# Kernel optimization log

Measured on AMD Instinct MI355X. Metric: run time of the kernel, lower is better.

The kernel has to match this reference:

```python
import jax, jax.numpy as jnp
import numpy as np
import math

DIM_IN = 512
DIM_OUT = 512
KERNEL = 3
STYLE_DIM = 2 * 128
LIN_SCALE = 1.0 / math.sqrt(STYLE_DIM)      # EqualLinear scale (lr_mul=1)
CONV_SCALE = 1.0 / math.sqrt(DIM_IN * KERNEL ** 2)  # fan_in = dim_in * k**2 (as in source)
PAD = KERNEL // 2


def setup_inputs() -> dict:
    key = jax.random.key(0)
    ks = jax.random.split(key, 5)
    B, T = 16, 2048
    x = jax.random.normal(ks[0], (B, DIM_IN, T), dtype=jnp.float32)
    c_src = jax.random.normal(ks[1], (B, 128), dtype=jnp.float32)
    c_trg = jax.random.normal(ks[2], (B, 128), dtype=jnp.float32)
    style_w = jax.random.normal(ks[3], (DIM_IN, STYLE_DIM), dtype=jnp.float32)
    style_b = jnp.ones((DIM_IN,), dtype=jnp.float32)  # bias_init=1
    weight = jax.random.normal(ks[4], (1, DIM_OUT, DIM_IN, KERNEL), dtype=jnp.float32)
    return {"x": x, "c_src": c_src, "c_trg": c_trg,
            "style_w": style_w, "style_b": style_b, "weight": weight}


def reference(x, c_src, c_trg, style_w, style_b, weight):
    B = x.shape[0]
    # EqualLinear: style code s [B, dim_in]
    c = jnp.concatenate([c_src, c_trg], axis=-1)              # [B, 256]
    s = c @ (style_w * LIN_SCALE).T + style_b                 # [B, dim_in]
    # Modulate: w [B, dim_out, dim_in, k]
    w = CONV_SCALE * weight * s[:, None, :, None]
    # Demodulate over (dim_in, k)
    demod = jax.lax.rsqrt(jnp.sum(w * w, axis=(2, 3)) + 1e-8)  # [B, dim_out]
    w = w * demod[:, :, None, None]
    # Per-sample conv1d, padding 'same' (pad = k//2), vmapped over batch
    def conv1(xi, wi):
        # xi: [dim_in, T], wi: [dim_out, dim_in, k]
        out = jax.lax.conv_general_dilated(
            xi[None], wi, window_strides=(1,), padding=[(PAD, PAD)],
            dimension_numbers=("NCH", "OIH", "NCH"))
        return out[0]                                          # [dim_out, T]
    return jax.vmap(conv1)(x, w)                               # [B, dim_out, T]
```

## Files before the change

### kernel.cpp

```cpp
#include <hip/hip_runtime.h>
#include <cstdint>
#include <cstddef>


#define LIN_SCALE  0.0625f
#define CONV_SCALE 0.014731391f

#define B_   16
#define CIN  512
#define COUT 512
#define T_   2048
#define TP   2050

typedef __bf16 bf16x8 __attribute__((ext_vector_type(8)));
typedef float  f32x4  __attribute__((ext_vector_type(4)));
typedef unsigned short u16x8 __attribute__((ext_vector_type(8)));
typedef unsigned short u16x2 __attribute__((ext_vector_type(2)));

__device__ inline unsigned short f2bf(float f) {
  __bf16 h = (__bf16)f;
  return __builtin_bit_cast(unsigned short, h);
}

__global__ __launch_bounds__(256) void style_kernel(const float* __restrict__ c_src,
                                                    const float* __restrict__ c_trg,
                                                    const float* __restrict__ sw,
                                                    const float* __restrict__ sb,
                                                    float* __restrict__ s) {
  __shared__ float c[256];
  const int b = blockIdx.y;
  const int tid = threadIdx.x;
  c[tid] = (tid < 128) ? c_src[b * 128 + tid] : c_trg[b * 128 + tid - 128];
  __syncthreads();
  const int w = tid >> 6, lane = tid & 63;
  #pragma unroll
  for (int rr = 0; rr < 16; ++rr) {
    const int i = blockIdx.x * 64 + w * 16 + rr;
    const float* row = sw + (size_t)i * 256;
    float acc = row[lane] * c[lane] + row[lane + 64] * c[lane + 64]
              + row[lane + 128] * c[lane + 128] + row[lane + 192] * c[lane + 192];
    #pragma unroll
    for (int off = 32; off; off >>= 1) acc += __shfl_down(acc, off, 64);
    if (lane == 0) s[b * 512 + i] = acc * LIN_SCALE + sb[i];
  }
}

__global__ __launch_bounds__(256) void modw_kernel(const float* __restrict__ weight,
                                                   const float* __restrict__ s,
                                                   unsigned short* __restrict__ Wm) {
  const int o = blockIdx.x;
  const int tid = threadIdx.x;
  __shared__ float wsh[1536];
  __shared__ float svs[16 * 512];
  __shared__ float partial[16][4];
  __shared__ float demv[16];

  #pragma unroll
  for (int j = tid; j < 1536; j += 256) wsh[j] = weight[(size_t)o * 1536 + j];
  #pragma unroll
  for (int j = tid; j < 16 * 512; j += 256) svs[j] = s[j];
  __syncthreads();

  float wr[6];
  #pragma unroll
  for (int q = 0; q < 6; ++q) wr[q] = wsh[tid * 6 + q] * CONV_SCALE;

  const int lane = tid & 63, w = tid >> 6;
  float ssb[16];
  #pragma unroll
  for (int b = 0; b < 16; ++b) {
    const float s0 = svs[b * 512 + 2 * tid];
    const float s1 = svs[b * 512 + 2 * tid + 1];
    float ss = 0.f;
    #pragma unroll
    for (int q = 0; q < 3; ++q) { float v = wr[q] * s0; ss += v * v; }
    #pragma unroll
    for (int q = 3; q < 6; ++q) { float v = wr[q] * s1; ss += v * v; }
    ssb[b] = ss;
  }
  #pragma unroll
  for (int b = 0; b < 16; ++b) {
    float ss = ssb[b];
    #pragma unroll
    for (int off = 32; off; off >>= 1) ss += __shfl_down(ss, off, 64);
    if (lane == 0) partial[b][w] = ss;
  }
  __syncthreads();
  if (tid < 16)
    demv[tid] = rsqrtf(partial[tid][0] + partial[tid][1] + partial[tid][2] + partial[tid][3] + 1e-8f);
  __syncthreads();

  #pragma unroll
  for (int b = 0; b < 16; ++b) {
    const float dem = demv[b];
    const float s0 = svs[b * 512 + 2 * tid] * dem;
    const float s1 = svs[b * 512 + 2 * tid + 1] * dem;
    #pragma unroll
    for (int k = 0; k < 3; ++k) {
      u16x2 v;
      v.x = f2bf(wr[k] * s0);
      v.y = f2bf(wr[3 + k] * s1);
      *(u16x2*)&Wm[(((size_t)b * 3 + k) * 512 + o) * 512 + 2 * tid] = v;
    }
  }
}

__global__ __launch_bounds__(256) void transpose_kernel(const float* __restrict__ x,
                                                        unsigned short* __restrict__ xT) {
  __shared__ float tile[64][65];
  const int b = blockIdx.z, i0 = blockIdx.y * 64, t0 = blockIdx.x * 64;
  const int tid = threadIdx.x;

  const int lr = tid >> 4;
  const int lc = (tid & 15) * 4;
  const float* xb = x + ((size_t)b * CIN + i0) * T_ + t0;
  #pragma unroll
  for (int p = 0; p < 4; ++p) {
    const int r = p * 16 + lr;
    const float4 v = *(const float4*)(xb + (size_t)r * T_ + lc);
    tile[r][lc + 0] = v.x; tile[r][lc + 1] = v.y;
    tile[r][lc + 2] = v.z; tile[r][lc + 3] = v.w;
  }
  if (blockIdx.x == 0 && tid < 8)
    *(u16x8*)&xT[(size_t)b * TP * CIN + i0 + tid * 8] = (u16x8){0,0,0,0,0,0,0,0};
  if (blockIdx.x == gridDim.x - 1 && tid < 8)
    *(u16x8*)&xT[((size_t)b * TP + TP - 1) * CIN + i0 + tid * 8] = (u16x8){0,0,0,0,0,0,0,0};
  __syncthreads();

  const int st = tid >> 3;
  const int si = (tid & 7) * 8;
  unsigned short* xTb = xT + ((size_t)b * TP + 1 + t0) * CIN + i0;
  #pragma unroll
  for (int p = 0; p < 2; ++p) {
    const int t = p * 32 + st;
    u16x8 v;
    #pragma unroll
    for (int q = 0; q < 8; ++q) v[q] = f2bf(tile[si + q][t]);
    *(u16x8*)&xTb[(size_t)t * CIN + si] = v;
  }
}

#define BM 64
#define BN 256
#define BK 64

__global__ __launch_bounds__(256, 2) void gemm_kernel(const unsigned short* __restrict__ Wm,
                                                      const unsigned short* __restrict__ xT,
                                                      float* __restrict__ out) {
  __shared__ unsigned short lA[3 * 64 * 64];
  __shared__ unsigned short lB[258 * 64];

  const int id  = blockIdx.x;
  const int xcd = id & 7;
  const int j   = id >> 3;
  const int b   = xcd + 8 * (j >> 6);
  const int r   = j & 63;
  const int o0  = (r >> 3) * BM;
  const int t0  = (r & 7) * BN;

  const int tid  = threadIdx.x;
  const int lane = tid & 63;
  const int wn   = (tid >> 6) * 64;

  const int srow  = tid >> 3;
  const int sxcol = ((tid & 7) ^ (srow & 7)) * 8;
  const unsigned short* gW = Wm + ((size_t)b * 3 * 512 + o0) * 512;
  const unsigned short* gX = xT + ((size_t)b * TP + t0) * CIN;

  f32x4 acc[4][4];
  #pragma unroll
  for (int i = 0; i < 4; ++i)
    #pragma unroll
    for (int jj = 0; jj < 4; ++jj) acc[i][jj] = (f32x4){0.f, 0.f, 0.f, 0.f};

  for (int kk = 0; kk < 8; ++kk) {
    const int i0 = kk * 64;
    __syncthreads();
    #pragma unroll
    for (int tap = 0; tap < 3; ++tap)
      #pragma unroll
      for (int p = 0; p < 2; ++p)
        __builtin_amdgcn_global_load_lds(
            (const __attribute__((address_space(1))) void*)
              (gW + (size_t)tap * 512 * 512 + (size_t)(p * 32 + srow) * 512 + i0 + sxcol),
            (__attribute__((address_space(3))) void*)(&lA[tap * 4096 + p * 2048 + tid * 8]),
            16, 0, 0);
    #pragma unroll
    for (int q = 0; q < 8; ++q)
      __builtin_amdgcn_global_load_lds(
          (const __attribute__((address_space(1))) void*)
            (gX + (size_t)(q * 32 + srow) * CIN + i0 + sxcol),
          (__attribute__((address_space(3))) void*)(&lB[(q * 256 + tid) * 8]),
          16, 0, 0);
    if (tid < 16)
      __builtin_amdgcn_global_load_lds(
          (const __attribute__((address_space(1))) void*)
            (gX + (size_t)(256 + srow) * CIN + i0 + sxcol),
          (__attribute__((address_space(3))) void*)(&lB[(2048 + tid) * 8]),
          16, 0, 0);
    __syncthreads();

    #pragma unroll
    for (int k = 0; k < 3; ++k) {
      #pragma unroll
      for (int s = 0; s < 2; ++s) {
        const int kc = s * 4 + (lane >> 4);
        bf16x8 af[4], bfr[4];
        #pragma unroll
        for (int mi = 0; mi < 4; ++mi) {
          const int ra = mi * 16 + (lane & 15);
          af[mi] = *(const bf16x8*)&lA[k * 4096 + ra * 64 + ((kc ^ (ra & 7)) << 3)];
        }
        #pragma unroll
        for (int ni = 0; ni < 4; ++ni) {
          const int rb = wn + ni * 16 + (lane & 15) + k;
          bfr[ni] = *(const bf16x8*)&lB[rb * 64 + ((kc ^ (rb & 7)) << 3)];
        }
        #pragma unroll
        for (int mi = 0; mi < 4; ++mi)
          #pragma unroll
          for (int ni = 0; ni < 4; ++ni)
            acc[mi][ni] = __builtin_amdgcn_mfma_f32_16x16x32_bf16(af[mi], bfr[ni], acc[mi][ni], 0, 0, 0);
      }
    }
  }

  float* ob = out + ((size_t)b * COUT + o0) * T_ + t0 + wn;
  const int rrow = (lane >> 4) * 4;
  const int ccol = lane & 15;
  #pragma unroll
  for (int mi = 0; mi < 4; ++mi)
    #pragma unroll
    for (int ni = 0; ni < 4; ++ni)
      #pragma unroll
      for (int rr = 0; rr < 4; ++rr)
        ob[(size_t)(mi * 16 + rrow + rr) * T_ + ni * 16 + ccol] = acc[mi][ni][rr];
}

extern "C" void kernel_launch(void* const* d_in, const int* in_sizes, int n_in,
                              void* d_out, int out_size, void* d_ws, size_t ws_size,
                              hipStream_t stream) {
  const float* x       = (const float*)d_in[0];
  const float* c_src   = (const float*)d_in[1];
  const float* c_trg   = (const float*)d_in[2];
  const float* style_w = (const float*)d_in[3];
  const float* style_b = (const float*)d_in[4];
  const float* weight  = (const float*)d_in[5];
  float* out = (float*)d_out;

  char* ws = (char*)d_ws;
  float* s_buf          = (float*)ws;
  unsigned short* Wm    = (unsigned short*)(ws + 32768);
  unsigned short* xTbuf = (unsigned short*)(ws + 32768 + 25165824);

  style_kernel<<<dim3(8, 16), 256, 0, stream>>>(c_src, c_trg, style_w, style_b, s_buf);
  modw_kernel<<<dim3(COUT), 256, 0, stream>>>(weight, s_buf, Wm);
  transpose_kernel<<<dim3(T_ / 64, CIN / 64, B_), 256, 0, stream>>>(x, xTbuf);
  gemm_kernel<<<dim3(1024), 256, 0, stream>>>(Wm, xTbuf, out);
}
```

Before: 188.9 us.

## Enlarge GEMM tile to 128x256 with 2x2 warp grid and BK=32

The modulated-conv GEMM block tile grows from 64x256 to 128x256, and each of the four waves now computes a 64x128 sub-tile instead of 64x64. K-step per LDS stage drops from 64 to 32 with a matching swizzle, and the grid halves to 512 blocks. This raises operand reuse per LDS load and lowers global traffic per output, at the cost of more accumulator registers (128 floats per thread), more K-loop barriers, and fewer blocks for occupancy.

```diff
diff --git a/kernel.cpp b/kernel.cpp
--- a/kernel.cpp
+++ b/kernel.cpp
@@ -16,6 +16,9 @@
 typedef float  f32x4  __attribute__((ext_vector_type(4)));
 typedef unsigned short u16x8 __attribute__((ext_vector_type(8)));
 typedef unsigned short u16x2 __attribute__((ext_vector_type(2)));
+
+#define AS1 __attribute__((address_space(1)))
+#define AS3 __attribute__((address_space(3)))
 
 __device__ inline unsigned short f2bf(float f) {
   __bf16 h = (__bf16)f;
@@ -140,98 +143,101 @@
   }
 }
 
-#define BM 64
+#define BM 128
 #define BN 256
-#define BK 64
+#define BK 32
 
 __global__ __launch_bounds__(256, 2) void gemm_kernel(const unsigned short* __restrict__ Wm,
                                                       const unsigned short* __restrict__ xT,
                                                       float* __restrict__ out) {
-  __shared__ unsigned short lA[3 * 64 * 64];
-  __shared__ unsigned short lB[258 * 64];
+  __shared__ unsigned short lA[3 * 128 * 32];
+  __shared__ unsigned short lB[258 * 32];
 
   const int id  = blockIdx.x;
   const int xcd = id & 7;
   const int j   = id >> 3;
-  const int b   = xcd + 8 * (j >> 6);
-  const int r   = j & 63;
+  const int b   = xcd + 8 * (j >> 5);
+  const int r   = j & 31;
   const int o0  = (r >> 3) * BM;
   const int t0  = (r & 7) * BN;
 
   const int tid  = threadIdx.x;
   const int lane = tid & 63;
-  const int wn   = (tid >> 6) * 64;
-
-  const int srow  = tid >> 3;
-  const int sxcol = ((tid & 7) ^ (srow & 7)) * 8;
+  const int wm   = ((tid >> 6) & 1) * 64;
+  const int wn   = (tid >> 7) * 128;
+  const int rl   = lane & 15;
+  const int kc   = lane >> 4;
+
   const unsigned short* gW = Wm + ((size_t)b * 3 * 512 + o0) * 512;
   const unsigned short* gX = xT + ((size_t)b * TP + t0) * CIN;
 
-  f32x4 acc[4][4];
+  f32x4 acc[4][8];
   #pragma unroll
   for (int i = 0; i < 4; ++i)
     #pragma unroll
-    for (int jj = 0; jj < 4; ++jj) acc[i][jj] = (f32x4){0.f, 0.f, 0.f, 0.f};
-
-  for (int kk = 0; kk < 8; ++kk) {
-    const int i0 = kk * 64;
+    for (int jj = 0; jj < 8; ++jj) acc[i][jj] = (f32x4){0.f, 0.f, 0.f, 0.f};
+
+  for (int kk = 0; kk < 16; ++kk) {
+    const int i0 = kk * 32;
     __syncthreads();
     #pragma unroll
-    for (int tap = 0; tap < 3; ++tap)
-      #pragma unroll
-      for (int p = 0; p < 2; ++p)
-        __builtin_amdgcn_global_load_lds(
-            (const __attribute__((address_space(1))) void*)
-              (gW + (size_t)tap * 512 * 512 + (size_t)(p * 32 + srow) * 512 + i0 + sxcol),
-            (__attribute__((address_space(3))) void*)(&lA[tap * 4096 + p * 2048 + tid * 8]),
-            16, 0, 0);
-    #pragma unroll
-    for (int q = 0; q < 8; ++q)
+    for (int q = 0; q < 6; ++q) {
+      const int ci  = q * 256 + tid;
+      const int row = ci >> 2;
+      const int tap = row >> 7;
+      const int ar  = row & 127;
+      const int gc  = ((ci & 3) ^ ((ar >> 1) & 3)) * 8;
       __builtin_amdgcn_global_load_lds(
-          (const __attribute__((address_space(1))) void*)
-            (gX + (size_t)(q * 32 + srow) * CIN + i0 + sxcol),
-          (__attribute__((address_space(3))) void*)(&lB[(q * 256 + tid) * 8]),
-          16, 0, 0);
-    if (tid < 16)
+          (const AS1 void*)(gW + (size_t)tap * 262144 + (size_t)ar * 512 + i0 + gc),
+          (AS3 void*)(&lA[ci * 8]), 16, 0, 0);
+    }
+    #pragma unroll
+    for (int q = 0; q < 4; ++q) {
+      const int ci  = q * 256 + tid;
+      const int row = ci >> 2;
+      const int gc  = ((ci & 3) ^ ((row >> 1) & 3)) * 8;
       __builtin_amdgcn_global_load_lds(
-          (const __attribute__((address_space(1))) void*)
-            (gX + (size_t)(256 + srow) * CIN + i0 + sxcol),
-          (__attribute__((address_space(3))) void*)(&lB[(2048 + tid) * 8]),
-          16, 0, 0);
+          (const AS1 void*)(gX + (size_t)row * CIN + i0 + gc),
+          (AS3 void*)(&lB[ci * 8]), 16, 0, 0);
+    }
+    if (tid < 8) {
+      const int ci  = 1024 + tid;
+      const int row = ci >> 2;
+      const int gc  = ((ci & 3) ^ ((row >> 1) & 3)) * 8;
+      __builtin_amdgcn_global_load_lds(
+          (const AS1 void*)(gX + (size_t)row * CIN + i0 + gc),
+          (AS3 void*)(&lB[ci * 8]), 16, 0, 0);
+    }
     __syncthreads();
 
     #pragma unroll
-    for (int k = 0; k < 3; ++k) {
-      #pragma unroll
-      for (int s = 0; s < 2; ++s) {
-        const int kc = s * 4 + (lane >> 4);
-        bf16x8 af[4], bfr[4];
+    for (int tap = 0; tap < 3; ++tap) {
+      bf16x8 af[4], bfr[8];
+      #pragma unroll
+      for (int mi = 0; mi < 4; ++mi) {
+        const int ra = wm + mi * 16 + rl;
+        af[mi] = *(const bf16x8*)&lA[((tap * 128 + ra) * 4 + (kc ^ ((ra >> 1) & 3))) * 8];
+      }
+      #pragma unroll
+      for (int ni = 0; ni < 8; ++ni) {
+        const int rb = wn + ni * 16 + rl + tap;
+        bfr[ni] = *(const bf16x8*)&lB[(rb * 4 + (kc ^ ((rb >> 1) & 3))) * 8];
+      }
+      #pragma unroll
+      for (int mi = 0; mi < 4; ++mi)
         #pragma unroll
-        for (int mi = 0; mi < 4; ++mi) {
-          const int ra = mi * 16 + (lane & 15);
-          af[mi] = *(const bf16x8*)&lA[k * 4096 + ra * 64 + ((kc ^ (ra & 7)) << 3)];
-        }
-        #pragma unroll
-        for (int ni = 0; ni < 4; ++ni) {
-          const int rb = wn + ni * 16 + (lane & 15) + k;
-          bfr[ni] = *(const bf16x8*)&lB[rb * 64 + ((kc ^ (rb & 7)) << 3)];
-        }
-        #pragma unroll
-        for (int mi = 0; mi < 4; ++mi)
-          #pragma unroll
-          for (int ni = 0; ni < 4; ++ni)
-            acc[mi][ni] = __builtin_amdgcn_mfma_f32_16x16x32_bf16(af[mi], bfr[ni], acc[mi][ni], 0, 0, 0);
-      }
-    }
-  }
-
-  float* ob = out + ((size_t)b * COUT + o0) * T_ + t0 + wn;
+        for (int ni = 0; ni < 8; ++ni)
+          acc[mi][ni] = __builtin_amdgcn_mfma_f32_16x16x32_bf16(af[mi], bfr[ni], acc[mi][ni], 0, 0, 0);
+    }
+  }
+
+  float* ob = out + ((size_t)b * COUT + o0 + wm) * T_ + t0 + wn;
   const int rrow = (lane >> 4) * 4;
   const int ccol = lane & 15;
   #pragma unroll
   for (int mi = 0; mi < 4; ++mi)
     #pragma unroll
-    for (int ni = 0; ni < 4; ++ni)
+    for (int ni = 0; ni < 8; ++ni)
       #pragma unroll
       for (int rr = 0; rr < 4; ++rr)
         ob[(size_t)(mi * 16 + rrow + rr) * T_ + ni * 16 + ccol] = acc[mi][ni][rr];
@@ -256,5 +262,5 @@
   style_kernel<<<dim3(8, 16), 256, 0, stream>>>(c_src, c_trg, style_w, style_b, s_buf);
   modw_kernel<<<dim3(COUT), 256, 0, stream>>>(weight, s_buf, Wm);
   transpose_kernel<<<dim3(T_ / 64, CIN / 64, B_), 256, 0, stream>>>(x, xTbuf);
-  gemm_kernel<<<dim3(1024), 256, 0, stream>>>(Wm, xTbuf, out);
-}
+  gemm_kernel<<<dim3(512), 256, 0, stream>>>(Wm, xTbuf, out);
+}
```

New measurement: 187.1 us. About the same (-1.0%).
